# Performance work log

Hardware: AMD Instinct MI355X
Metric: run time of the kernel (lower is better)

The kernel has to match this reference:

```python
import jax, jax.numpy as jnp
import numpy as np

S, B, D = 2048, 16, 512  # seq_len, batch, dim_in (= value_dim = key_dim)


def setup_inputs() -> dict:
    key = jax.random.key(0)
    ks = jax.random.split(key, 7)
    scale = 1.0 / np.sqrt(D)
    return {
        "seq": jax.random.normal(ks[0], (S, B, D), dtype=jnp.float32),
        "Wv": jax.random.normal(ks[1], (D, D), dtype=jnp.float32) * scale,
        "bv": jax.random.normal(ks[2], (D,), dtype=jnp.float32) * 0.01,
        "Wq": jax.random.normal(ks[3], (D, D), dtype=jnp.float32) * scale,
        "bq": jax.random.normal(ks[4], (D,), dtype=jnp.float32) * 0.01,
        "Wk": jax.random.normal(ks[5], (D, D), dtype=jnp.float32) * scale,
        "bk": jax.random.normal(ks[6], (D,), dtype=jnp.float32) * 0.01,
    }


def reference(seq, Wv, bv, Wq, bq, Wk, bk):
    # seq: [S, B, D] -> [B, S, D]
    x = jnp.transpose(seq, (1, 0, 2))
    value = x @ Wv.T + bv   # [B, S, Dv]
    query = x @ Wq.T + bq   # [B, S, Dv]
    keys = x @ Wk.T + bk    # [B, S, Dk]
    inv_sqrt_d = 1.0 / np.sqrt(seq.shape[-1]).astype(np.float32)
    # note: scores use value @ query^T (roles swapped vs standard SDPA), per source
    weights = jnp.einsum('bsd,btd->bst', value, query) * inv_sqrt_d  # [B, S, S]
    weights = jax.nn.softmax(weights, axis=-1)
    out = jnp.einsum('bst,btk->bsk', weights, keys)  # [B, S, Dk]
    return jnp.transpose(out, (1, 0, 2))  # [S, B, Dk]
```

## Files before the change

kernel.cpp:

```cpp
#include <hip/hip_runtime.h>
#include <hip/hip_bf16.h>

#define SS 2048
#define BB 16
#define DD 512

typedef __attribute__((ext_vector_type(4))) float f32x4;
typedef __attribute__((ext_vector_type(8))) short bf16x8;
typedef __attribute__((ext_vector_type(4))) unsigned short us4;
typedef unsigned short us;

#define MFMA16(a,b,c) __builtin_amdgcn_mfma_f32_16x16x32_bf16((a),(b),(c),0,0,0)
#define BAR() __builtin_amdgcn_s_barrier()
#define WAITV(n) asm volatile("s_waitcnt vmcnt(" #n ")" ::: "memory")
#define WAITL()  asm volatile("s_waitcnt lgkmcnt(0)" ::: "memory")
#define ADV(s) s = ((s) == 2 ? 0 : (s) + 1)

__device__ __forceinline__ unsigned short f2b(float f) {
    union { float f; unsigned u; } v; v.f = f;
    unsigned r = v.u + 0x7FFFu + ((v.u >> 16) & 1u);
    return (unsigned short)(r >> 16);
}

__device__ __forceinline__ bf16x8 ldfrag8(const us* base, int row, int kelem) {
    int off = (row << 8) + (kelem << 1);
    off ^= (row & 15) << 4;
    return *(const bf16x8*)((const char*)base + off);
}
__device__ __forceinline__ bf16x8 ldfrag(const us* base, int row, int kelem, int rowshift) {
    int off = (row << rowshift) + (kelem << 1);
    off ^= (row & 7) << 4;
    return *(const bf16x8*)((const char*)base + off);
}

__device__ __forceinline__ void gl16(const void* g, void* l) {
    __builtin_amdgcn_global_load_lds(
        (const __attribute__((address_space(1))) unsigned*)g,
        (__attribute__((address_space(3))) unsigned*)l, 16, 0, 0);
}

__global__ __launch_bounds__(256) void k_prep_x(const float* __restrict__ seq,
        us* __restrict__ Xb, us* __restrict__ Xbt) {
    __shared__ __align__(16) char L[64 * 128];
    const int tid = threadIdx.x;
    const int d0 = blockIdx.x * 64, s0 = blockIdx.y * 64, b = blockIdx.z;
    {
        int r = tid >> 2, seg = (tid & 3) * 16;
        const float* src = seq + (size_t)(s0 + r) * (BB * DD) + (size_t)b * DD + d0 + seg;
        __align__(16) us vals[16];
        #pragma unroll
        for (int q = 0; q < 4; ++q) {
            f32x4 v = *(const f32x4*)(src + q * 4);
            vals[q*4+0] = f2b(v.x); vals[q*4+1] = f2b(v.y);
            vals[q*4+2] = f2b(v.z); vals[q*4+3] = f2b(v.w);
        }
        us* xo = Xb + ((size_t)b * SS + s0 + r) * DD + d0 + seg;
        *(bf16x8*)xo       = *(bf16x8*)&vals[0];
        *(bf16x8*)(xo + 8) = *(bf16x8*)&vals[8];
        #pragma unroll
        for (int j = 0; j < 16; ++j) {
            int d = seg + j;
            int addr = (d * 128 + r * 2) ^ ((d & 7) << 4);
            *(us*)(L + addr) = vals[j];
        }
    }
    __syncthreads();
    {
        int d = tid >> 2, sseg = (tid & 3) * 16;
        int c = (d & 7) << 4;
        int base = d * 128 + sseg * 2;
        bf16x8 h0 = *(bf16x8*)(L + (base ^ c));
        bf16x8 h1 = *(bf16x8*)(L + ((base + 16) ^ c));
        us* o = Xbt + ((size_t)b * DD + d0 + d) * SS + s0 + sseg;
        *(bf16x8*)o       = h0;
        *(bf16x8*)(o + 8) = h1;
    }
}

__global__ __launch_bounds__(256) void k_prepG(const float* __restrict__ Wv,
        const float* __restrict__ Wq, us* __restrict__ Gt) {
    __shared__ float Sq[32][64], Sv[32][64];
    const int tid = threadIdx.x;
    const int p0 = blockIdx.x * 64, i0 = blockIdx.y * 64;
    const int tp = tid & 15, ti = tid >> 4;
    float acc[4][4] = {};
    for (int a0 = 0; a0 < DD; a0 += 32) {
        #pragma unroll
        for (int j = 0; j < 2; ++j) {
            int slot = tid + j * 256;
            int row = slot >> 4, c4 = (slot & 15) * 4;
            *(f32x4*)&Sq[row][c4] = *(const f32x4*)(Wq + (size_t)(a0 + row) * DD + p0 + c4);
            *(f32x4*)&Sv[row][c4] = *(const f32x4*)(Wv + (size_t)(a0 + row) * DD + i0 + c4);
        }
        __syncthreads();
        for (int a = 0; a < 32; ++a) {
            f32x4 q = *(f32x4*)&Sq[a][tp * 4];
            f32x4 v = *(f32x4*)&Sv[a][ti * 4];
            #pragma unroll
            for (int x = 0; x < 4; ++x)
                #pragma unroll
                for (int y = 0; y < 4; ++y)
                    acc[x][y] += q[x] * v[y];
        }
        __syncthreads();
    }
    const float sc = 0.044194173824159216f;
    #pragma unroll
    for (int x = 0; x < 4; ++x)
        #pragma unroll
        for (int y = 0; y < 4; ++y)
            Gt[(size_t)(p0 + tp * 4 + x) * DD + i0 + ti * 4 + y] = f2b(acc[x][y] * sc);
}

__global__ __launch_bounds__(512) void k_prepU(const float* __restrict__ Wq,
        const float* __restrict__ bv, float* __restrict__ u) {
    int p = threadIdx.x;
    float s = 0.f;
    for (int a0 = 0; a0 < DD; a0 += 8) {
        #pragma unroll
        for (int j = 0; j < 8; ++j)
            s += bv[a0 + j] * Wq[(size_t)(a0 + j) * DD + p];
    }
    u[p] = s * 0.044194173824159216f;
}

__global__ void k_prepW(const float* __restrict__ Wk, us* __restrict__ Wkb) {
    int i = (blockIdx.x * 256 + threadIdx.x) * 4;
    f32x4 v = *(const f32x4*)(Wk + i);
    us4 o; o.x = f2b(v.x); o.y = f2b(v.y); o.z = f2b(v.z); o.w = f2b(v.w);
    *(us4*)(Wkb + i) = o;
}

template<int OUTMODE>
__global__ __launch_bounds__(256, 2) void k_gemm(
        const us* __restrict__ A, const us* __restrict__ Bm,
        const float* __restrict__ bias, void* __restrict__ outp) {
    __shared__ __align__(16) us As[2][128 * 64];
    __shared__ __align__(16) us Bs[2][128 * 64];
    const int tid = threadIdx.x;
    const int lane = tid & 63;
    const int w = tid >> 6;
    const int wr = w >> 1, wc = w & 1;
    const int l15 = lane & 15, lg = lane >> 4;
    const int b = blockIdx.x >> 4;
    const int s0 = (blockIdx.x & 15) * 128;
    const int n0 = blockIdx.y * 128;
    const char* abase = (const char*)(A + ((size_t)b * SS + s0) * DD);
    const char* bbase = (const char*)Bm + (size_t)n0 * 1024;

    f32x4 acc[4][4];
    #pragma unroll
    for (int m = 0; m < 4; ++m)
        #pragma unroll
        for (int n = 0; n < 4; ++n) acc[m][n] = (f32x4)(0.0f);

    auto stage = [&](int db, int p) {
        #pragma unroll
        for (int j = 0; j < 4; ++j) {
            int x = (tid + j * 256) * 16;
            int gx = x ^ (((x >> 7) & 7) << 4);
            int row = gx >> 7, col = gx & 127;
            gl16(abase + (size_t)row * 1024 + p * 128 + col, (char*)As[db] + x);
            gl16(bbase + (size_t)row * 1024 + p * 128 + col, (char*)Bs[db] + x);
        }
    };

    stage(0, 0);
    for (int p = 0; p < 8; ++p) {
        if (p < 7) { stage((p + 1) & 1, p + 1); WAITV(8); }
        else       { WAITV(0); }
        BAR();
        const us* Ac = As[p & 1]; const us* Bc = Bs[p & 1];
        __builtin_amdgcn_s_setprio(1);
        #pragma unroll
        for (int kk = 0; kk < 2; ++kk) {
            bf16x8 af[4], bfr[4];
            #pragma unroll
            for (int m = 0; m < 4; ++m) af[m]  = ldfrag(Ac, 64 * wr + 16 * m + l15, kk * 32 + 8 * lg, 7);
            #pragma unroll
            for (int n = 0; n < 4; ++n) bfr[n] = ldfrag(Bc, 64 * wc + 16 * n + l15, kk * 32 + 8 * lg, 7);
            #pragma unroll
            for (int m = 0; m < 4; ++m)
                #pragma unroll
                for (int n = 0; n < 4; ++n)
                    acc[m][n] = MFMA16(af[m], bfr[n], acc[m][n]);
        }
        __builtin_amdgcn_s_setprio(0);
        BAR();
    }

    #pragma unroll
    for (int m = 0; m < 4; ++m) {
        #pragma unroll
        for (int n = 0; n < 4; ++n) {
            int col = n0 + 64 * wc + 16 * n + l15;
            float bia = bias[col];
            #pragma unroll
            for (int r = 0; r < 4; ++r) {
                int row = s0 + 64 * wr + 16 * m + 4 * lg + r;
                float v = acc[m][n][r] + bia;
                if (OUTMODE == 0)
                    ((us*)outp)[((size_t)b * SS + row) * DD + col] = f2b(v);
                else
                    ((float*)outp)[((size_t)row * BB + b) * DD + col] = v;
            }
        }
    }
}

__global__ __launch_bounds__(512, 2) void k_attn(
        const us* __restrict__ Vtb, const us* __restrict__ Xb,
        const us* __restrict__ Xbt, us* __restrict__ Ob) {
    __shared__ __align__(16) us BUFS[3][16384];
    __shared__ __align__(16) us Pb[64 * 128];
    __shared__ float red[2][64];

    const int tid = threadIdx.x;
    const int lane = tid & 63;
    const int w = tid >> 6;
    const int rg = w & 3;
    const int cg = w >> 2;
    const int l15 = lane & 15, lg = lane >> 4;

    const int wg = blockIdx.x;
    const int b  = wg & 15;
    const int s0 = (wg >> 4) * 64;

    const char* vbase  = (const char*)(Vtb + ((size_t)b * SS + s0) * DD);
    const char* xabase = (const char*)(Xb  + (size_t)b * SS * DD);
    const char* xtbase = (const char*)(Xbt + (size_t)b * DD * SS);

    auto issue = [&](int cflat, us* dst0) {
        int c = cflat & 127;
        int i = c & 7, t0 = (c >> 3) << 7;
        char* dst = (char*)dst0;
        if (i < 4) {
            #pragma unroll
            for (int j = 0; j < 4; ++j) {
                int x = tid * 16 + j * 8192;
                int gx = x ^ (((x >> 8) & 15) << 4);
                int row = gx >> 8, col = gx & 255;
                gl16(xabase + (size_t)(t0 + row) * 1024 + i * 256 + col, dst + x);
            }
        } else {
            #pragma unroll
            for (int j = 0; j < 4; ++j) {
                int x = tid * 16 + j * 8192;
                int gx = x ^ (((x >> 8) & 15) << 4);
                int row = gx >> 8, col = gx & 255;
                gl16(xtbase + (size_t)((i - 4) * 128 + row) * (SS * 2)
                            + (size_t)t0 * 2 + col, dst + x);
            }
        }
    };

    #pragma unroll
    for (int p = 0; p < 4; ++p) {
        #pragma unroll
        for (int j = 0; j < 2; ++j) {
            int x = tid * 16 + j * 8192;
            int gx = x ^ (((x >> 8) & 15) << 4);
            int row = gx >> 8, col = gx & 255;
            gl16(vbase + (size_t)row * 1024 + p * 256 + col,
                 (char*)BUFS[0] + p * 16384 + x);
        }
    }
    WAITV(0); BAR();
    bf16x8 af[16];
    #pragma unroll
    for (int p = 0; p < 4; ++p)
        #pragma unroll
        for (int kk = 0; kk < 4; ++kk)
            af[4 * p + kk] = ldfrag8((const us*)BUFS[0] + p * 8192,
                                     16 * rg + l15, 32 * kk + 8 * lg);
    WAITL(); BAR();

    int wslot = 0, rslot = 0;
    issue(0, BUFS[wslot]); ADV(wslot);
    issue(1, BUFS[wslot]); ADV(wslot);

    f32x4 accv[4][4];
    #pragma unroll
    for (int ph = 0; ph < 4; ++ph)
        #pragma unroll
        for (int nt = 0; nt < 4; ++nt) accv[ph][nt] = (f32x4)(0.0f);
    float lsum[4] = {0.f, 0.f, 0.f, 0.f};
    const int idx = 16 * rg + 4 * lg;

    for (int step = 0; step < 16; ++step) {
        const int cbase = step * 8;
        f32x4 sacc[4];
        #pragma unroll
        for (int nt = 0; nt < 4; ++nt) sacc[nt] = (f32x4)(0.0f);

        #pragma unroll
        for (int p = 0; p < 4; ++p) {
            issue(cbase + p + 2, BUFS[wslot]); ADV(wslot);
            WAITV(8); BAR();
            const us* sl = BUFS[rslot]; ADV(rslot);
            __builtin_amdgcn_s_setprio(1);
            #pragma unroll
            for (int kk = 0; kk < 4; ++kk)
                #pragma unroll
                for (int nt = 0; nt < 4; ++nt) {
                    bf16x8 bq = ldfrag8(sl, 64 * cg + 16 * nt + l15, 32 * kk + 8 * lg);
                    sacc[nt] = MFMA16(af[4 * p + kk], bq, sacc[nt]);
                }
            __builtin_amdgcn_s_setprio(0);
            BAR();
        }

        #pragma unroll
        for (int nt = 0; nt < 4; ++nt)
            #pragma unroll
            for (int ri = 0; ri < 4; ++ri)
                sacc[nt][ri] = __expf(sacc[nt][ri]);
        #pragma unroll
        for (int nt = 0; nt < 4; ++nt)
            #pragma unroll
            for (int ri = 0; ri < 4; ++ri) {
                int row = idx + ri;
                int col = 64 * cg + 16 * nt + l15;
                int off = ((row << 8) + (col << 1)) ^ ((row & 15) << 4);
                *(us*)((char*)Pb + off) = f2b(sacc[nt][ri]);
            }
        #pragma unroll
        for (int ri = 0; ri < 4; ++ri) {
            float s = sacc[0][ri] + sacc[1][ri] + sacc[2][ri] + sacc[3][ri];
            s += __shfl_xor(s, 1); s += __shfl_xor(s, 2);
            s += __shfl_xor(s, 4); s += __shfl_xor(s, 8);
            lsum[ri] += s;
        }
        WAITL(); BAR();
        bf16x8 pa[4];
        #pragma unroll
        for (int kk = 0; kk < 4; ++kk)
            pa[kk] = ldfrag8(Pb, 16 * rg + l15, 32 * kk + 8 * lg);

        #pragma unroll
        for (int p = 0; p < 4; ++p) {
            issue(cbase + p + 6, BUFS[wslot]); ADV(wslot);
            WAITV(8); BAR();
            const us* sl = BUFS[rslot]; ADV(rslot);
            __builtin_amdgcn_s_setprio(1);
            #pragma unroll
            for (int kk = 0; kk < 4; ++kk)
                #pragma unroll
                for (int nt = 0; nt < 4; ++nt) {
                    bf16x8 bx = ldfrag8(sl, 64 * cg + 16 * nt + l15, 32 * kk + 8 * lg);
                    accv[p][nt] = MFMA16(pa[kk], bx, accv[p][nt]);
                }
            __builtin_amdgcn_s_setprio(0);
            BAR();
        }
    }

    if (l15 == 0) {
        #pragma unroll
        for (int ri = 0; ri < 4; ++ri)
            red[cg][idx + ri] = lsum[ri];
    }
    WAITL(); BAR();
    float tot[4];
    #pragma unroll
    for (int ri = 0; ri < 4; ++ri)
        tot[ri] = red[0][idx + ri] + red[1][idx + ri];
    us* orow = Ob + ((size_t)b * SS + s0) * DD;
    #pragma unroll
    for (int ph = 0; ph < 4; ++ph)
        #pragma unroll
        for (int nt = 0; nt < 4; ++nt)
            #pragma unroll
            for (int ri = 0; ri < 4; ++ri) {
                int row = idx + ri;
                int e = 128 * ph + 64 * cg + 16 * nt + l15;
                orow[(size_t)row * DD + e] = f2b(accv[ph][nt][ri] / tot[ri]);
            }
}

extern "C" void kernel_launch(void* const* d_in, const int* in_sizes, int n_in,
                              void* d_out, int out_size, void* d_ws, size_t ws_size,
                              hipStream_t stream) {
    const float* seq = (const float*)d_in[0];
    const float* Wv  = (const float*)d_in[1];
    const float* bv  = (const float*)d_in[2];
    const float* Wq  = (const float*)d_in[3];
    const float* Wk  = (const float*)d_in[5];
    const float* bk  = (const float*)d_in[6];

    char* ws = (char*)d_ws;
    us*    Xb  = (us*)ws;
    us*    Xbt = (us*)(ws + (size_t)33554432);
    us*    Vtb = (us*)(ws + (size_t)67108864);
    us*    Gt  = (us*)(ws + (size_t)100663296);
    us*    Wkb = (us*)(ws + (size_t)101187584);
    float* u   = (float*)(ws + (size_t)101711872);

    k_prep_x<<<dim3(8, 32, 16), 256, 0, stream>>>(seq, Xb, Xbt);
    k_prepG<<<dim3(8, 8), 256, 0, stream>>>(Wv, Wq, Gt);
    k_prepU<<<1, 512, 0, stream>>>(Wq, bv, u);
    k_prepW<<<256, 256, 0, stream>>>(Wk, Wkb);

    k_gemm<0><<<dim3(256, 4), 256, 0, stream>>>(Xb, Gt, u, (void*)Vtb);
    k_attn<<<512, 512, 0, stream>>>(Vtb, Xb, Xbt, Vtb);
    k_gemm<1><<<dim3(256, 4), 256, 0, stream>>>(Vtb, Wkb, bk, d_out);
}
```

Before: 377.3 us.

## Switch attention kernel to 32x32x16 MFMA with 2x4 warp grid and MFMA row sums

Reorganizes the attention kernel's 8 waves from a 4x2 to a 2x4 row/column grid. Both score and PV products now use 32x32x16 bf16 MFMA tiles instead of 16x16x32, which cuts LDS fragment loads per MFMA. Softmax row sums are computed by multiplying the bf16 P tile with a ones vector on the MFMA unit, replacing shuffle reductions and the final cross-wave LDS reduction. To hold the larger A-fragment set in registers, the last quarter of the V tile stays in a new LDS buffer and is reloaded each step. This raises register and LDS pressure, and the row sums now come from bf16-rounded P rather than fp32 values.

```diff
diff --git a/kernel.cpp b/kernel.cpp
--- a/kernel.cpp
+++ b/kernel.cpp
@@ -6,11 +6,13 @@
 #define DD 512
 
 typedef __attribute__((ext_vector_type(4))) float f32x4;
+typedef __attribute__((ext_vector_type(16))) float f32x16;
 typedef __attribute__((ext_vector_type(8))) short bf16x8;
 typedef __attribute__((ext_vector_type(4))) unsigned short us4;
 typedef unsigned short us;
 
 #define MFMA16(a,b,c) __builtin_amdgcn_mfma_f32_16x16x32_bf16((a),(b),(c),0,0,0)
+#define MFMA32(a,b,c) __builtin_amdgcn_mfma_f32_32x32x16_bf16((a),(b),(c),0,0,0)
 #define BAR() __builtin_amdgcn_s_barrier()
 #define WAITV(n) asm volatile("s_waitcnt vmcnt(" #n ")" ::: "memory")
 #define WAITL()  asm volatile("s_waitcnt lgkmcnt(0)" ::: "memory")
@@ -212,15 +214,15 @@
         const us* __restrict__ Vtb, const us* __restrict__ Xb,
         const us* __restrict__ Xbt, us* __restrict__ Ob) {
     __shared__ __align__(16) us BUFS[3][16384];
+    __shared__ __align__(16) us VtL[64 * 128];
     __shared__ __align__(16) us Pb[64 * 128];
-    __shared__ float red[2][64];
 
     const int tid = threadIdx.x;
     const int lane = tid & 63;
     const int w = tid >> 6;
-    const int rg = w & 3;
-    const int cg = w >> 2;
-    const int l15 = lane & 15, lg = lane >> 4;
+    const int rg = w & 1;
+    const int cg = w >> 1;
+    const int l31 = lane & 31, lh = lane >> 5;
 
     const int wg = blockIdx.x;
     const int b  = wg & 15;
@@ -256,42 +258,40 @@
 
     #pragma unroll
     for (int p = 0; p < 4; ++p) {
+        char* dst = (p < 3) ? (char*)BUFS[p] : (char*)VtL;
         #pragma unroll
         for (int j = 0; j < 2; ++j) {
             int x = tid * 16 + j * 8192;
             int gx = x ^ (((x >> 8) & 15) << 4);
             int row = gx >> 8, col = gx & 255;
-            gl16(vbase + (size_t)row * 1024 + p * 256 + col,
-                 (char*)BUFS[0] + p * 16384 + x);
+            gl16(vbase + (size_t)row * 1024 + p * 256 + col, dst + x);
         }
     }
     WAITV(0); BAR();
-    bf16x8 af[16];
-    #pragma unroll
-    for (int p = 0; p < 4; ++p)
-        #pragma unroll
-        for (int kk = 0; kk < 4; ++kk)
-            af[4 * p + kk] = ldfrag8((const us*)BUFS[0] + p * 8192,
-                                     16 * rg + l15, 32 * kk + 8 * lg);
+    bf16x8 af[24];
+    #pragma unroll
+    for (int p = 0; p < 3; ++p)
+        #pragma unroll
+        for (int ks = 0; ks < 8; ++ks)
+            af[8 * p + ks] = ldfrag8(BUFS[p], 32 * rg + l31, 16 * ks + 8 * lh);
     WAITL(); BAR();
 
     int wslot = 0, rslot = 0;
     issue(0, BUFS[wslot]); ADV(wslot);
     issue(1, BUFS[wslot]); ADV(wslot);
 
-    f32x4 accv[4][4];
-    #pragma unroll
-    for (int ph = 0; ph < 4; ++ph)
-        #pragma unroll
-        for (int nt = 0; nt < 4; ++nt) accv[ph][nt] = (f32x4)(0.0f);
-    float lsum[4] = {0.f, 0.f, 0.f, 0.f};
-    const int idx = 16 * rg + 4 * lg;
+    const short one_bf = (short)0x3F80;
+    const bf16x8 ones = {one_bf, one_bf, one_bf, one_bf,
+                         one_bf, one_bf, one_bf, one_bf};
+
+    f32x16 accv[4];
+    #pragma unroll
+    for (int j = 0; j < 4; ++j) accv[j] = (f32x16)(0.0f);
+    f32x16 lsumv = (f32x16)(0.0f);
 
     for (int step = 0; step < 16; ++step) {
         const int cbase = step * 8;
-        f32x4 sacc[4];
-        #pragma unroll
-        for (int nt = 0; nt < 4; ++nt) sacc[nt] = (f32x4)(0.0f);
+        f32x16 sacc = (f32x16)(0.0f);
 
         #pragma unroll
         for (int p = 0; p < 4; ++p) {
@@ -300,42 +300,35 @@
             const us* sl = BUFS[rslot]; ADV(rslot);
             __builtin_amdgcn_s_setprio(1);
             #pragma unroll
-            for (int kk = 0; kk < 4; ++kk)
-                #pragma unroll
-                for (int nt = 0; nt < 4; ++nt) {
-                    bf16x8 bq = ldfrag8(sl, 64 * cg + 16 * nt + l15, 32 * kk + 8 * lg);
-                    sacc[nt] = MFMA16(af[4 * p + kk], bq, sacc[nt]);
-                }
+            for (int ks = 0; ks < 8; ++ks) {
+                bf16x8 a = (p < 3) ? af[8 * p + ks]
+                                   : ldfrag8(VtL, 32 * rg + l31, 16 * ks + 8 * lh);
+                bf16x8 bq = ldfrag8(sl, 32 * cg + l31, 16 * ks + 8 * lh);
+                sacc = MFMA32(a, bq, sacc);
+            }
             __builtin_amdgcn_s_setprio(0);
             BAR();
         }
 
         #pragma unroll
-        for (int nt = 0; nt < 4; ++nt)
-            #pragma unroll
-            for (int ri = 0; ri < 4; ++ri)
-                sacc[nt][ri] = __expf(sacc[nt][ri]);
-        #pragma unroll
-        for (int nt = 0; nt < 4; ++nt)
-            #pragma unroll
-            for (int ri = 0; ri < 4; ++ri) {
-                int row = idx + ri;
-                int col = 64 * cg + 16 * nt + l15;
-                int off = ((row << 8) + (col << 1)) ^ ((row & 15) << 4);
-                *(us*)((char*)Pb + off) = f2b(sacc[nt][ri]);
-            }
-        #pragma unroll
-        for (int ri = 0; ri < 4; ++ri) {
-            float s = sacc[0][ri] + sacc[1][ri] + sacc[2][ri] + sacc[3][ri];
-            s += __shfl_xor(s, 1); s += __shfl_xor(s, 2);
-            s += __shfl_xor(s, 4); s += __shfl_xor(s, 8);
-            lsum[ri] += s;
+        for (int r = 0; r < 16; ++r)
+            sacc[r] = __expf(sacc[r]);
+        #pragma unroll
+        for (int r = 0; r < 16; ++r) {
+            int row = 32 * rg + (r & 3) + 8 * (r >> 2) + 4 * lh;
+            int col = 32 * cg + l31;
+            int off = ((row << 8) + (col << 1)) ^ ((row & 15) << 4);
+            *(us*)((char*)Pb + off) = f2b(sacc[r]);
         }
         WAITL(); BAR();
-        bf16x8 pa[4];
-        #pragma unroll
-        for (int kk = 0; kk < 4; ++kk)
-            pa[kk] = ldfrag8(Pb, 16 * rg + l15, 32 * kk + 8 * lg);
+
+        bf16x8 pa[8];
+        #pragma unroll
+        for (int ts = 0; ts < 8; ++ts)
+            pa[ts] = ldfrag8(Pb, 32 * rg + l31, 16 * ts + 8 * lh);
+        #pragma unroll
+        for (int ts = 0; ts < 8; ++ts)
+            lsumv = MFMA32(pa[ts], ones, lsumv);
 
         #pragma unroll
         for (int p = 0; p < 4; ++p) {
@@ -344,38 +337,24 @@
             const us* sl = BUFS[rslot]; ADV(rslot);
             __builtin_amdgcn_s_setprio(1);
             #pragma unroll
-            for (int kk = 0; kk < 4; ++kk)
-                #pragma unroll
-                for (int nt = 0; nt < 4; ++nt) {
-                    bf16x8 bx = ldfrag8(sl, 64 * cg + 16 * nt + l15, 32 * kk + 8 * lg);
-                    accv[p][nt] = MFMA16(pa[kk], bx, accv[p][nt]);
-                }
+            for (int ts = 0; ts < 8; ++ts) {
+                bf16x8 bx = ldfrag8(sl, 32 * cg + l31, 16 * ts + 8 * lh);
+                accv[p] = MFMA32(pa[ts], bx, accv[p]);
+            }
             __builtin_amdgcn_s_setprio(0);
             BAR();
         }
     }
 
-    if (l15 == 0) {
-        #pragma unroll
-        for (int ri = 0; ri < 4; ++ri)
-            red[cg][idx + ri] = lsum[ri];
-    }
-    WAITL(); BAR();
-    float tot[4];
-    #pragma unroll
-    for (int ri = 0; ri < 4; ++ri)
-        tot[ri] = red[0][idx + ri] + red[1][idx + ri];
     us* orow = Ob + ((size_t)b * SS + s0) * DD;
     #pragma unroll
-    for (int ph = 0; ph < 4; ++ph)
-        #pragma unroll
-        for (int nt = 0; nt < 4; ++nt)
-            #pragma unroll
-            for (int ri = 0; ri < 4; ++ri) {
-                int row = idx + ri;
-                int e = 128 * ph + 64 * cg + 16 * nt + l15;
-                orow[(size_t)row * DD + e] = f2b(accv[ph][nt][ri] / tot[ri]);
-            }
+    for (int j = 0; j < 4; ++j)
+        #pragma unroll
+        for (int r = 0; r < 16; ++r) {
+            int row = 32 * rg + (r & 3) + 8 * (r >> 2) + 4 * lh;
+            int e = 128 * j + 32 * cg + l31;
+            orow[(size_t)row * DD + e] = f2b(accv[j][r] / lsumv[r]);
+        }
 }
 
 extern "C" void kernel_launch(void* const* d_in, const int* in_sizes, int n_in,
```

Result: slower. 435.9 us (+15.5%).

## Restructure attention pipeline into two 64KB half-buffers and compute row sums via MFMA

Applied to the files above, without the earlier changes.

Replaces the triple-buffered 32KB LDS ring with two 64KB buffers that each hold half of the K or V tile. Each step now does 4 large compute phases with fewer barriers, issuing the next load into a buffer right after it is consumed. The softmax row-sum shuffle reduction and the cross-wave LDS reduction are replaced by MFMAs of the bf16 probabilities against a ones vector. LDS use per block grows (128KB plus Pb), which may limit occupancy to one block per CU despite launch_bounds(512,2), and prefetch distance is only one phase.

```diff
diff --git a/kernel.cpp b/kernel.cpp
--- a/kernel.cpp
+++ b/kernel.cpp
@@ -14,7 +14,6 @@
 #define BAR() __builtin_amdgcn_s_barrier()
 #define WAITV(n) asm volatile("s_waitcnt vmcnt(" #n ")" ::: "memory")
 #define WAITL()  asm volatile("s_waitcnt lgkmcnt(0)" ::: "memory")
-#define ADV(s) s = ((s) == 2 ? 0 : (s) + 1)
 
 __device__ __forceinline__ unsigned short f2b(float f) {
     union { float f; unsigned u; } v; v.f = f;
@@ -25,6 +24,11 @@
 __device__ __forceinline__ bf16x8 ldfrag8(const us* base, int row, int kelem) {
     int off = (row << 8) + (kelem << 1);
     off ^= (row & 15) << 4;
+    return *(const bf16x8*)((const char*)base + off);
+}
+__device__ __forceinline__ bf16x8 ldfrag9(const us* base, int row, int kelem) {
+    int off = (row << 9) + (kelem << 1);
+    off ^= (row & 15) << 5;
     return *(const bf16x8*)((const char*)base + off);
 }
 __device__ __forceinline__ bf16x8 ldfrag(const us* base, int row, int kelem, int rowshift) {
@@ -211,9 +215,8 @@
 __global__ __launch_bounds__(512, 2) void k_attn(
         const us* __restrict__ Vtb, const us* __restrict__ Xb,
         const us* __restrict__ Xbt, us* __restrict__ Ob) {
-    __shared__ __align__(16) us BUFS[3][16384];
+    __shared__ __align__(16) us XW[2][32768];
     __shared__ __align__(16) us Pb[64 * 128];
-    __shared__ float red[2][64];
 
     const int tid = threadIdx.x;
     const int lane = tid & 63;
@@ -230,27 +233,25 @@
     const char* xabase = (const char*)(Xb  + (size_t)b * SS * DD);
     const char* xtbase = (const char*)(Xbt + (size_t)b * DD * SS);
 
-    auto issue = [&](int cflat, us* dst0) {
-        int c = cflat & 127;
-        int i = c & 7, t0 = (c >> 3) << 7;
+    auto issueX = [&](int h, int t0, us* dst0) {
         char* dst = (char*)dst0;
-        if (i < 4) {
-            #pragma unroll
-            for (int j = 0; j < 4; ++j) {
-                int x = tid * 16 + j * 8192;
-                int gx = x ^ (((x >> 8) & 15) << 4);
-                int row = gx >> 8, col = gx & 255;
-                gl16(xabase + (size_t)(t0 + row) * 1024 + i * 256 + col, dst + x);
-            }
-        } else {
-            #pragma unroll
-            for (int j = 0; j < 4; ++j) {
-                int x = tid * 16 + j * 8192;
-                int gx = x ^ (((x >> 8) & 15) << 4);
-                int row = gx >> 8, col = gx & 255;
-                gl16(xtbase + (size_t)((i - 4) * 128 + row) * (SS * 2)
-                            + (size_t)t0 * 2 + col, dst + x);
-            }
+        #pragma unroll
+        for (int j = 0; j < 8; ++j) {
+            int x = tid * 16 + j * 8192;
+            int gx = x ^ (((x >> 9) & 15) << 5);
+            int row = gx >> 9, col = gx & 511;
+            gl16(xabase + (size_t)(t0 + row) * 1024 + h * 512 + col, dst + x);
+        }
+    };
+    auto issueT = [&](int h, int t0, us* dst0) {
+        char* dst = (char*)dst0;
+        #pragma unroll
+        for (int j = 0; j < 8; ++j) {
+            int x = tid * 16 + j * 8192;
+            int gx = x ^ (((x >> 8) & 15) << 4);
+            int row = gx >> 8, col = gx & 255;
+            gl16(xtbase + (size_t)(h * 256 + row) * (SS * 2)
+                        + (size_t)t0 * 2 + col, dst + x);
         }
     };
 
@@ -262,7 +263,7 @@
             int gx = x ^ (((x >> 8) & 15) << 4);
             int row = gx >> 8, col = gx & 255;
             gl16(vbase + (size_t)row * 1024 + p * 256 + col,
-                 (char*)BUFS[0] + p * 16384 + x);
+                 (char*)XW[0] + p * 16384 + x);
         }
     }
     WAITV(0); BAR();
@@ -271,44 +272,57 @@
     for (int p = 0; p < 4; ++p)
         #pragma unroll
         for (int kk = 0; kk < 4; ++kk)
-            af[4 * p + kk] = ldfrag8((const us*)BUFS[0] + p * 8192,
+            af[4 * p + kk] = ldfrag8((const us*)XW[0] + p * 8192,
                                      16 * rg + l15, 32 * kk + 8 * lg);
     WAITL(); BAR();
 
-    int wslot = 0, rslot = 0;
-    issue(0, BUFS[wslot]); ADV(wslot);
-    issue(1, BUFS[wslot]); ADV(wslot);
-
-    f32x4 accv[4][4];
-    #pragma unroll
-    for (int ph = 0; ph < 4; ++ph)
-        #pragma unroll
-        for (int nt = 0; nt < 4; ++nt) accv[ph][nt] = (f32x4)(0.0f);
-    float lsum[4] = {0.f, 0.f, 0.f, 0.f};
+    issueX(0, 0, XW[0]);
+    issueX(1, 0, XW[1]);
+
+    const short one_bf = (short)0x3F80;
+    const bf16x8 ones = {one_bf, one_bf, one_bf, one_bf,
+                         one_bf, one_bf, one_bf, one_bf};
+
+    f32x4 accv[2][8];
+    #pragma unroll
+    for (int h = 0; h < 2; ++h)
+        #pragma unroll
+        for (int nt = 0; nt < 8; ++nt) accv[h][nt] = (f32x4)(0.0f);
+    f32x4 lsum = (f32x4)(0.0f);
     const int idx = 16 * rg + 4 * lg;
 
     for (int step = 0; step < 16; ++step) {
-        const int cbase = step * 8;
+        const int t0 = step * 128;
+        const int t0n = (t0 + 128) & (SS - 1);
         f32x4 sacc[4];
         #pragma unroll
         for (int nt = 0; nt < 4; ++nt) sacc[nt] = (f32x4)(0.0f);
 
-        #pragma unroll
-        for (int p = 0; p < 4; ++p) {
-            issue(cbase + p + 2, BUFS[wslot]); ADV(wslot);
-            WAITV(8); BAR();
-            const us* sl = BUFS[rslot]; ADV(rslot);
-            __builtin_amdgcn_s_setprio(1);
-            #pragma unroll
-            for (int kk = 0; kk < 4; ++kk)
-                #pragma unroll
-                for (int nt = 0; nt < 4; ++nt) {
-                    bf16x8 bq = ldfrag8(sl, 64 * cg + 16 * nt + l15, 32 * kk + 8 * lg);
-                    sacc[nt] = MFMA16(af[4 * p + kk], bq, sacc[nt]);
-                }
-            __builtin_amdgcn_s_setprio(0);
-            BAR();
-        }
+        WAITV(8); BAR();
+        __builtin_amdgcn_s_setprio(1);
+        #pragma unroll
+        for (int kk = 0; kk < 8; ++kk)
+            #pragma unroll
+            for (int nt = 0; nt < 4; ++nt) {
+                bf16x8 bq = ldfrag9(XW[0], 64 * cg + 16 * nt + l15, 32 * kk + 8 * lg);
+                sacc[nt] = MFMA16(af[kk], bq, sacc[nt]);
+            }
+        __builtin_amdgcn_s_setprio(0);
+        BAR();
+        issueT(0, t0, XW[0]);
+
+        WAITV(8); BAR();
+        __builtin_amdgcn_s_setprio(1);
+        #pragma unroll
+        for (int kk = 0; kk < 8; ++kk)
+            #pragma unroll
+            for (int nt = 0; nt < 4; ++nt) {
+                bf16x8 bq = ldfrag9(XW[1], 64 * cg + 16 * nt + l15, 32 * kk + 8 * lg);
+                sacc[nt] = MFMA16(af[8 + kk], bq, sacc[nt]);
+            }
+        __builtin_amdgcn_s_setprio(0);
+        BAR();
+        issueT(1, t0, XW[1]);
 
         #pragma unroll
         for (int nt = 0; nt < 4; ++nt)
@@ -324,57 +338,52 @@
                 int off = ((row << 8) + (col << 1)) ^ ((row & 15) << 4);
                 *(us*)((char*)Pb + off) = f2b(sacc[nt][ri]);
             }
-        #pragma unroll
-        for (int ri = 0; ri < 4; ++ri) {
-            float s = sacc[0][ri] + sacc[1][ri] + sacc[2][ri] + sacc[3][ri];
-            s += __shfl_xor(s, 1); s += __shfl_xor(s, 2);
-            s += __shfl_xor(s, 4); s += __shfl_xor(s, 8);
-            lsum[ri] += s;
-        }
         WAITL(); BAR();
         bf16x8 pa[4];
         #pragma unroll
         for (int kk = 0; kk < 4; ++kk)
             pa[kk] = ldfrag8(Pb, 16 * rg + l15, 32 * kk + 8 * lg);
-
-        #pragma unroll
-        for (int p = 0; p < 4; ++p) {
-            issue(cbase + p + 6, BUFS[wslot]); ADV(wslot);
-            WAITV(8); BAR();
-            const us* sl = BUFS[rslot]; ADV(rslot);
-            __builtin_amdgcn_s_setprio(1);
-            #pragma unroll
-            for (int kk = 0; kk < 4; ++kk)
-                #pragma unroll
-                for (int nt = 0; nt < 4; ++nt) {
-                    bf16x8 bx = ldfrag8(sl, 64 * cg + 16 * nt + l15, 32 * kk + 8 * lg);
-                    accv[p][nt] = MFMA16(pa[kk], bx, accv[p][nt]);
-                }
-            __builtin_amdgcn_s_setprio(0);
-            BAR();
-        }
-    }
-
-    if (l15 == 0) {
-        #pragma unroll
-        for (int ri = 0; ri < 4; ++ri)
-            red[cg][idx + ri] = lsum[ri];
-    }
-    WAITL(); BAR();
-    float tot[4];
-    #pragma unroll
-    for (int ri = 0; ri < 4; ++ri)
-        tot[ri] = red[0][idx + ri] + red[1][idx + ri];
+        #pragma unroll
+        for (int kk = 0; kk < 4; ++kk)
+            lsum = MFMA16(pa[kk], ones, lsum);
+
+        WAITV(8); BAR();
+        __builtin_amdgcn_s_setprio(1);
+        #pragma unroll
+        for (int kk = 0; kk < 4; ++kk)
+            #pragma unroll
+            for (int nt = 0; nt < 8; ++nt) {
+                bf16x8 bx = ldfrag8(XW[0], 128 * cg + 16 * nt + l15, 32 * kk + 8 * lg);
+                accv[0][nt] = MFMA16(pa[kk], bx, accv[0][nt]);
+            }
+        __builtin_amdgcn_s_setprio(0);
+        BAR();
+        issueX(0, t0n, XW[0]);
+
+        WAITV(8); BAR();
+        __builtin_amdgcn_s_setprio(1);
+        #pragma unroll
+        for (int kk = 0; kk < 4; ++kk)
+            #pragma unroll
+            for (int nt = 0; nt < 8; ++nt) {
+                bf16x8 bx = ldfrag8(XW[1], 128 * cg + 16 * nt + l15, 32 * kk + 8 * lg);
+                accv[1][nt] = MFMA16(pa[kk], bx, accv[1][nt]);
+            }
+        __builtin_amdgcn_s_setprio(0);
+        BAR();
+        issueX(1, t0n, XW[1]);
+    }
+
     us* orow = Ob + ((size_t)b * SS + s0) * DD;
     #pragma unroll
-    for (int ph = 0; ph < 4; ++ph)
-        #pragma unroll
-        for (int nt = 0; nt < 4; ++nt)
+    for (int h = 0; h < 2; ++h)
+        #pragma unroll
+        for (int nt = 0; nt < 8; ++nt)
             #pragma unroll
             for (int ri = 0; ri < 4; ++ri) {
                 int row = idx + ri;
-                int e = 128 * ph + 64 * cg + 16 * nt + l15;
-                orow[(size_t)row * DD + e] = f2b(accv[ph][nt][ri] / tot[ri]);
+                int e = 256 * h + 128 * cg + 16 * nt + l15;
+                orow[(size_t)row * DD + e] = f2b(accv[h][nt][ri] / lsum[ri]);
             }
 }
 
```

Result: slower. 428.8 us (+13.6%).
